# Kernel optimization log

Hardware: AMD Instinct MI355X
Metric: run time of the kernel (lower is better)

Reference implementation:

```python
import jax, jax.numpy as jnp
import numpy as np
from jax import lax

B, DIM, H, W = 8, 128, 64, 64
CQ, DI, DS, RK = 32, 64, 16, 2  # quarter dim, d_inner=2*CQ, d_state, dt_rank=ceil(32/16)
EPS = 1e-5


def _dw(x, w, dil):
    # depthwise conv, x: [B,C,H,W], w: [C,1,kh,kw], torch padding='same'
    return lax.conv_general_dilated(x, w, (1, 1), 'SAME', rhs_dilation=(dil, dil),
                                    dimension_numbers=('NCHW', 'OIHW', 'NCHW'),
                                    feature_group_count=x.shape[1])


def _ln(x, g, b):
    mu = jnp.mean(x, -1, keepdims=True)
    v = jnp.mean((x - mu) ** 2, -1, keepdims=True)
    return (x - mu) * lax.rsqrt(v + EPS) * g + b


def _bn_eval(x, g, b):
    # BatchNorm2d eval mode with default running stats (mean 0, var 1)
    return x * lax.rsqrt(jnp.float32(1.0) + EPS) * g[None, :, None, None] + b[None, :, None, None]


def _axial_dw(x, kh, kw, k3, g, b, dil):
    y = _dw(x, kw, dil)   # (1,w) mixer
    y = _dw(y, kh, dil)   # (h,1) mixer
    y = _dw(y, k3, dil)   # 3x3 dw
    return _bn_eval(y, g, b) + x


def _vss(x, ln_g, ln_b, in_w, conv_w, conv_b, xproj_w, dtw, dtb, A_logs, Ds, on_g, on_b, out_w):
    # x: [B,H,W,CQ] channels-last; VMamba VSSBlock: x + SS2D(LN(x))
    Bb, Hh, Ww, _ = x.shape
    L = Hh * Ww
    xz = _ln(x, ln_g, ln_b) @ in_w.T                      # [B,H,W,2*DI]
    xw, z = jnp.split(xz, 2, axis=-1)
    xc = jax.nn.silu(_dw(xw.transpose(0, 3, 1, 2), conv_w, 1) + conv_b[None, :, None, None])
    xf = xc.reshape(Bb, DI, L)                            # row-major scan
    xwh = xc.transpose(0, 1, 3, 2).reshape(Bb, DI, L)     # column-major scan
    xs = jnp.stack([xf, xwh, jnp.flip(xf, -1), jnp.flip(xwh, -1)], axis=1)  # [B,4,DI,L]
    x_dbl = jnp.einsum('bkdl,kcd->bkcl', xs, xproj_w)     # [B,4,RK+2*DS,L]
    delta = jax.nn.softplus(jnp.einsum('bkrl,kdr->bkdl', x_dbl[:, :, :RK], dtw) + dtb[None, :, :, None])
    Bs, Cs = x_dbl[:, :, RK:RK + DS], x_dbl[:, :, RK + DS:]
    A = -jnp.exp(A_logs)                                  # [4,DI,DS]

    def step(h, t):
        u, d, Bt, Ct = t                                  # u,d:[B,4,DI]; Bt,Ct:[B,4,DS]
        h = h * jnp.exp(d[..., None] * A) + (d * u)[..., None] * Bt[:, :, None, :]
        return h, jnp.einsum('bkdn,bkn->bkd', h, Ct)

    seq = (xs.transpose(3, 0, 1, 2), delta.transpose(3, 0, 1, 2),
           Bs.transpose(3, 0, 1, 2), Cs.transpose(3, 0, 1, 2))
    _, ys = lax.scan(step, jnp.zeros((Bb, 4, DI, DS), x.dtype), seq)  # [L,B,4,DI]
    ys = ys.transpose(1, 2, 3, 0) + Ds[None, :, :, None] * xs         # [B,4,DI,L]
    y = ys[:, 0] + jnp.flip(ys[:, 2], -1)
    y_wh = ys[:, 1] + jnp.flip(ys[:, 3], -1)
    y = y + y_wh.reshape(Bb, DI, Ww, Hh).transpose(0, 1, 3, 2).reshape(Bb, DI, L)
    y = _ln(y.reshape(Bb, DI, Hh, Ww).transpose(0, 2, 3, 1), on_g, on_b)
    return x + (y * jax.nn.silu(z)) @ out_w.T


def _forward(x, dw1_kh, dw1_kw, dw1_k3, dw1_g, dw1_b, dw2_kh, dw2_kw, dw2_k3, dw2_g, dw2_b,
             dw3_kh, dw3_kw, dw3_k3, dw3_g, dw3_b, ln_g, ln_b, in_w, conv_w, conv_b, xproj_w,
             dtw, dtb, A_logs, Ds, on_g, on_b, out_w, scale1, scale2, scale3, scale4, bn_g, bn_b):
    x1, x2, x3, x4 = jnp.split(x, 4, axis=1)
    vp = (ln_g, ln_b, in_w, conv_w, conv_b, xproj_w, dtw, dtb, A_logs, Ds, on_g, on_b, out_w)

    def branch(xi, kh, kw, k3, g, b, dil, s):
        y = _axial_dw(xi, kh, kw, k3, g, b, dil)
        y = _vss(y.transpose(0, 2, 3, 1), *vp).transpose(0, 3, 1, 2)
        return y * s

    y1 = branch(x1, dw1_kh, dw1_kw, dw1_k3, dw1_g, dw1_b, 1, scale1)
    y2 = branch(x2, dw2_kh, dw2_kw, dw2_k3, dw2_g, dw2_b, 2, scale2)
    y3 = branch(x3, dw3_kh, dw3_kw, dw3_k3, dw3_g, dw3_b, 3, scale3)
    y4 = x4 * scale4
    return jax.nn.relu(_bn_eval(jnp.concatenate([y1, y2, y3, y4], 1), bn_g, bn_b))


def setup_inputs():
    ks = jax.random.split(jax.random.key(0), 40)
    rn = lambda k, s, sc: jax.random.normal(k, s, jnp.float32) * sc
    inp = {'x': jax.random.normal(ks[0], (B, DIM, H, W), jnp.float32)}
    for i, n in enumerate(['dw1', 'dw2', 'dw3']):
        inp[n + '_kh'] = rn(ks[1 + 3 * i], (CQ, 1, 7, 1), 0.2)
        inp[n + '_kw'] = rn(ks[2 + 3 * i], (CQ, 1, 1, 7), 0.2)
        inp[n + '_k3'] = rn(ks[3 + 3 * i], (CQ, 1, 3, 3), 0.2)
        inp[n + '_g'] = jnp.ones((CQ,))
        inp[n + '_b'] = jnp.zeros((CQ,))
    inp['ln_g'] = jnp.ones((CQ,))
    inp['ln_b'] = jnp.zeros((CQ,))
    inp['in_w'] = rn(ks[10], (2 * DI, CQ), 0.1)
    inp['conv_w'] = rn(ks[11], (DI, 1, 3, 3), 0.2)
    inp['conv_b'] = jnp.zeros((DI,))
    inp['xproj_w'] = rn(ks[12], (4, RK + 2 * DS, DI), 0.1)
    inp['dtw'] = rn(ks[13], (4, DI, RK), 0.5)
    inp['dtb'] = rn(ks[14], (4, DI), 0.5)
    inp['A_logs'] = jnp.log(jnp.broadcast_to(jnp.arange(1, DS + 1, dtype=jnp.float32), (4, DI, DS)))
    inp['Ds'] = jnp.ones((4, DI))
    inp['on_g'] = jnp.ones((DI,))
    inp['on_b'] = jnp.zeros((DI,))
    inp['out_w'] = rn(ks[15], (CQ, DI), 0.1)
    for n in ['scale1', 'scale2', 'scale3', 'scale4']:
        inp[n] = jnp.ones((1,))
    inp['bn_g'] = jnp.ones((DIM,))
    inp['bn_b'] = jnp.zeros((DIM,))
    return inp


def reference(x, dw1_kh, dw1_kw, dw1_k3, dw1_g, dw1_b, dw2_kh, dw2_kw, dw2_k3, dw2_g, dw2_b,
              dw3_kh, dw3_kw, dw3_k3, dw3_g, dw3_b, ln_g, ln_b, in_w, conv_w, conv_b, xproj_w,
              dtw, dtb, A_logs, Ds, on_g, on_b, out_w, scale1, scale2, scale3, scale4, bn_g, bn_b):
    return _forward(x, dw1_kh, dw1_kw, dw1_k3, dw1_g, dw1_b, dw2_kh, dw2_kw, dw2_k3, dw2_g, dw2_b,
                    dw3_kh, dw3_kw, dw3_k3, dw3_g, dw3_b, ln_g, ln_b, in_w, conv_w, conv_b, xproj_w,
                    dtw, dtb, A_logs, Ds, on_g, on_b, out_w, scale1, scale2, scale3, scale4, bn_g, bn_b)
```

## Files before the change

### kernel.cpp

```cpp
#include <hip/hip_runtime.h>
#include <hip/hip_bf16.h>
#include <cstdint>

typedef unsigned short ushort_t;
typedef float f32x2 __attribute__((ext_vector_type(2)));

__device__ __forceinline__ float softplus2(float x){
    return fmaxf(x, 0.f) + __logf(1.f + __expf(-fabsf(x)));
}
__device__ __forceinline__ float siluf(float x){
    return x / (1.f + __expf(-x));
}
__device__ __forceinline__ float b2f(ushort_t u){
    union { uint32_t i; float f; } v; v.i = ((uint32_t)u)<<16; return v.f;
}
__device__ __forceinline__ ushort_t f2b(float f){
    uint32_t x = __float_as_uint(f);
    uint32_t r = (x + 0x7FFFu + ((x>>16)&1u)) >> 16;
    return (ushort_t)r;
}

struct AxialParams {
    const float* kh[3]; const float* kw[3]; const float* k3[3];
    const float* g[3];  const float* b[3];
};

__global__ __launch_bounds__(256) void k_axial(const float* __restrict__ x,
                                               float* __restrict__ Y0, AxialParams P){
    __shared__ float s0[4096];
    __shared__ float s1[4096];
    int bid = blockIdx.x;
    int i = bid >> 8;
    int rem = bid & 255;
    int b = rem >> 5, c = rem & 31;
    int dil = i + 1;
    const float* xin = x + ((size_t)(b*128 + i*32 + c))*4096;
    float wkw[7], wkh[7], wk3[9];
    #pragma unroll
    for(int t=0;t<7;t++){ wkw[t]=P.kw[i][c*7+t]; wkh[t]=P.kh[i][c*7+t]; }
    #pragma unroll
    for(int t=0;t<9;t++) wk3[t]=P.k3[i][c*9+t];
    float gc = P.g[i][c], bc = P.b[i][c];
    int tid = threadIdx.x;
    for(int idx=tid; idx<4096; idx+=256) s0[idx]=xin[idx];
    __syncthreads();
    for(int idx=tid; idx<4096; idx+=256){
        int h=idx>>6, w=idx&63; float a=0.f;
        #pragma unroll
        for(int t=0;t<7;t++){ int ww=w+(t-3)*dil; if(ww>=0&&ww<64) a=fmaf(s0[h*64+ww],wkw[t],a); }
        s1[idx]=a;
    }
    __syncthreads();
    for(int idx=tid; idx<4096; idx+=256){
        int h=idx>>6, w=idx&63; float a=0.f;
        #pragma unroll
        for(int t=0;t<7;t++){ int hh=h+(t-3)*dil; if(hh>=0&&hh<64) a=fmaf(s1[hh*64+w],wkh[t],a); }
        s0[idx]=a;
    }
    __syncthreads();
    const float inv = rsqrtf(1.00001f);
    float* out = Y0 + ((size_t)(i*8+b)*32 + c)*4096;
    for(int idx=tid; idx<4096; idx+=256){
        int h=idx>>6, w=idx&63; float a=0.f;
        #pragma unroll
        for(int t=0;t<9;t++){
            int hh=h+((t/3)-1)*dil, ww=w+((t%3)-1)*dil;
            if(hh>=0&&hh<64&&ww>=0&&ww<64) a=fmaf(s0[hh*64+ww],wk3[t],a);
        }
        out[idx] = a*inv*gc + bc + xin[idx];
    }
}

__global__ __launch_bounds__(256) void k_lnproj(const float* __restrict__ Y0,
        const float* __restrict__ ln_g, const float* __restrict__ ln_b,
        const float* __restrict__ in_w, ushort_t* __restrict__ XW, ushort_t* __restrict__ ZS){
    __shared__ float W[128*32];
    int tid=threadIdx.x;
    for(int idx=tid; idx<4096; idx+=256) W[idx]=in_w[idx];
    __syncthreads();
    int pg = blockIdx.x*256 + tid;
    int ib = pg>>12, p = pg&4095;
    const float* src = Y0 + (size_t)ib*32*4096;
    float t[32];
    float mu=0.f;
    #pragma unroll
    for(int c=0;c<32;c++){ t[c]=src[c*4096+p]; mu+=t[c]; }
    mu *= (1.f/32.f);
    float v=0.f;
    #pragma unroll
    for(int c=0;c<32;c++){ float d=t[c]-mu; v+=d*d; }
    v *= (1.f/32.f);
    float rs = rsqrtf(v+1e-5f);
    #pragma unroll
    for(int c=0;c<32;c++) t[c] = (t[c]-mu)*rs*ln_g[c] + ln_b[c];
    ushort_t* xw = XW + (size_t)ib*64*4096 + p;
    ushort_t* zs = ZS + (size_t)ib*64*4096 + p;
    for(int j=0;j<64;j++){
        float a=0.f, a2=0.f;
        #pragma unroll
        for(int c=0;c<32;c++){
            a  = fmaf(t[c], W[j*32+c],      a);
            a2 = fmaf(t[c], W[(j+64)*32+c], a2);
        }
        xw[(size_t)j*4096] = f2b(a);
        zs[(size_t)j*4096] = f2b(siluf(a2));
    }
}

__global__ __launch_bounds__(256) void k_dwt(const ushort_t* __restrict__ XW,
        const float* __restrict__ cw, const float* __restrict__ cb,
        ushort_t* __restrict__ XC, ushort_t* __restrict__ XCT){
    __shared__ ushort_t sin_[4096];
    __shared__ ushort_t tr[64*66];
    int bid=blockIdx.x, tid=threadIdx.x;
    int d = bid&63;
    const ushort_t* src = XW + (size_t)bid*4096;
    for(int idx=tid; idx<1024; idx+=256)
        *reinterpret_cast<ushort4*>(&sin_[idx*4]) = *reinterpret_cast<const ushort4*>(&src[idx*4]);
    float wk[9];
    #pragma unroll
    for(int t=0;t<9;t++) wk[t]=cw[d*9+t];
    float bias=cb[d];
    __syncthreads();
    ushort_t* outp = XC + (size_t)bid*4096;
    for(int idx=tid; idx<4096; idx+=256){
        int h=idx>>6, wq=idx&63;
        float a=bias;
        #pragma unroll
        for(int t=0;t<9;t++){
            int hh=h+(t/3)-1, ww=wq+(t%3)-1;
            if(hh>=0&&hh<64&&ww>=0&&ww<64) a=fmaf(b2f(sin_[hh*64+ww]),wk[t],a);
        }
        ushort_t vb = f2b(siluf(a));
        outp[idx]=vb;
        tr[wq*66+h]=vb;
    }
    __syncthreads();
    ushort_t* outt = XCT + (size_t)bid*4096;
    for(int idx=tid; idx<4096; idx+=256){
        outt[idx]=tr[(idx>>6)*66+(idx&63)];
    }
}

__global__ __launch_bounds__(256) void k_transpose(const ushort_t* __restrict__ src, ushort_t* __restrict__ dst){
    __shared__ ushort_t tile[64*66];
    size_t plane = blockIdx.x;
    const ushort_t* s = src + plane*4096;
    ushort_t* d = dst + plane*4096;
    int tid=threadIdx.x;
    for(int idx=tid; idx<4096; idx+=256){
        int h=idx>>6, w=idx&63;
        tile[w*66+h]=s[idx];
    }
    __syncthreads();
    for(int idx=tid; idx<4096; idx+=256){
        d[idx]=tile[(idx>>6)*66 + (idx&63)];
    }
}

__global__ __launch_bounds__(256) void k_xdbl(const ushort_t* __restrict__ XC, const ushort_t* __restrict__ XCT,
        const float* __restrict__ xproj, ushort_t* __restrict__ XBb, ushort_t* __restrict__ XCc,
        float* __restrict__ DT){
    __shared__ float Wt[64][36];
    int bid=blockIdx.x; int tid=threadIdx.x;
    int ibk = bid>>4; int lb = bid&15;
    int k = ibk & 3; int ib = ibk>>2;
    for(int idx=tid; idx<2176; idx+=256){
        int c=idx>>6, dd=idx&63;
        Wt[dd][c]=xproj[k*2176+idx];
    }
    __syncthreads();
    int l = lb*256+tid;
    const ushort_t* src = ((k&1)?XCT:XC) + (size_t)ib*64*4096;
    int idxl = (k&2)? (4095-l) : l;
    float acc[34];
    #pragma unroll
    for(int c=0;c<34;c++) acc[c]=0.f;
    for(int dd=0;dd<64;dd++){
        float u = b2f(src[(size_t)dd*4096 + idxl]);
        float wv[36];
        const float4* wp = reinterpret_cast<const float4*>(&Wt[dd][0]);
        *reinterpret_cast<float4*>(&wv[0])  = wp[0];
        *reinterpret_cast<float4*>(&wv[4])  = wp[1];
        *reinterpret_cast<float4*>(&wv[8])  = wp[2];
        *reinterpret_cast<float4*>(&wv[12]) = wp[3];
        *reinterpret_cast<float4*>(&wv[16]) = wp[4];
        *reinterpret_cast<float4*>(&wv[20]) = wp[5];
        *reinterpret_cast<float4*>(&wv[24]) = wp[6];
        *reinterpret_cast<float4*>(&wv[28]) = wp[7];
        *reinterpret_cast<float2*>(&wv[32]) = *reinterpret_cast<const float2*>(&Wt[dd][32]);
        #pragma unroll
        for(int c=0;c<34;c++) acc[c] = fmaf(u, wv[c], acc[c]);
    }
    DT[((size_t)ibk*2)*4096 + l]   = acc[0];
    DT[((size_t)ibk*2+1)*4096 + l] = acc[1];
    ushort_t* ob = XBb + ((size_t)ibk*16)*4096 + l;
    ushort_t* oc = XCc + ((size_t)ibk*16)*4096 + l;
    #pragma unroll
    for(int c=0;c<16;c++){
        ob[(size_t)c*4096]=f2b(acc[2+c]);
        oc[(size_t)c*4096]=f2b(acc[18+c]);
    }
}


template<bool UNI>
__device__ __forceinline__ void scan1_body(int w,int d,float dt0,float dt1,float db,
    const float* An, f32x2* h2, float& S,
    const float (*sB)[64][16], const float (*sdt)[64][2], const ushort_t (*su)[66])
{
    for(int s=0;s<64;s++){
        const float* dp=&sdt[w][s][0];
        float delta=softplus2(fmaf(dt0,dp[0],fmaf(dt1,dp[1],db)));
        S+=delta;
        int j = w? 63-s : s;
        float du = delta*b2f(su[j][d]);
        float bb[16];
        const float4* bp=reinterpret_cast<const float4*>(&sB[w][s][0]);
        reinterpret_cast<float4*>(bb)[0]=bp[0];
        reinterpret_cast<float4*>(bb)[1]=bp[1];
        reinterpret_cast<float4*>(bb)[2]=bp[2];
        reinterpret_cast<float4*>(bb)[3]=bp[3];
        if(UNI){
            float r1=__expf(delta*An[0]);
            f32x2 a={r1,r1*r1}, rq={r1*r1,r1*r1}, du2={du,du};
            const f32x2* b2p=reinterpret_cast<const f32x2*>(bb);
            #pragma unroll
            for(int i=0;i<8;i++){ h2[i]=h2[i]*a+du2*b2p[i]; a=a*rq; }
        } else {
            float* hf=reinterpret_cast<float*>(h2);
            #pragma unroll
            for(int n=0;n<16;n++){ float a=__expf(delta*An[n]); hf[n]=fmaf(hf[n],a,du*bb[n]); }
        }
    }
}

__global__ __launch_bounds__(128) void k_scan1(const ushort_t* __restrict__ XBb, const float* __restrict__ DT,
        const ushort_t* __restrict__ XC, const ushort_t* __restrict__ XCT,
        const float* __restrict__ dtw, const float* __restrict__ dtb,
        const float* __restrict__ A_logs,
        ushort_t* __restrict__ CHS, float* __restrict__ SD){
    __shared__ float sB[2][64][16];
    __shared__ float sdt[2][64][2];
    __shared__ ushort_t su[64][66];
    int bid=blockIdx.x, tid=threadIdx.x;
    int ib = bid>>7; int rem = bid&127; int p = rem>>6; int ch = rem&63;
    int w = tid>>6, d = tid&63;
    int l0 = ch*64, r0 = 4032 - l0;
    const ushort_t* B0 = XBb + (size_t)(4*ib+p)*16*4096;
    const ushort_t* B1 = XBb + (size_t)(4*ib+p+2)*16*4096;
    for(int idx=tid; idx<512; idx+=128){
        int w2=idx>>8, n=(idx>>4)&15, q=(idx&15)*4;
        const ushort_t* Bs = w2? B1 : B0;
        int base = (w2? r0 : l0) + q;
        ushort4 v = *reinterpret_cast<const ushort4*>(&Bs[(size_t)n*4096 + base]);
        sB[w2][q+0][n]=b2f(v.x); sB[w2][q+1][n]=b2f(v.y); sB[w2][q+2][n]=b2f(v.z); sB[w2][q+3][n]=b2f(v.w);
    }
    {
        const float* D0 = DT + (size_t)(4*ib+p)*2*4096;
        const float* D1 = DT + (size_t)(4*ib+p+2)*2*4096;
        int r=tid>>6, s=tid&63;
        sdt[0][s][r] = D0[(size_t)r*4096 + l0 + s];
        sdt[1][s][r] = D1[(size_t)r*4096 + r0 + s];
    }
    const ushort_t* U = (p?XCT:XC) + (size_t)ib*64*4096;
    for(int idx=tid; idx<1024; idx+=128){
        int r=idx>>4, q=(idx&15)*4;
        ushort4 v = *reinterpret_cast<const ushort4*>(&U[(size_t)r*4096 + l0 + q]);
        su[q+0][r]=v.x; su[q+1][r]=v.y; su[q+2][r]=v.z; su[q+3][r]=v.w;
    }
    __syncthreads();
    int k = p + 2*w;
    float dt0=dtw[(k*64+d)*2], dt1=dtw[(k*64+d)*2+1], db=dtb[k*64+d];
    float An[16];
    #pragma unroll
    for(int n=0;n<16;n++) An[n] = -__expf(A_logs[(k*64+d)*16+n]);
    bool st = true;
    #pragma unroll
    for(int n=1;n<16;n++) st = st && (fabsf(An[n]-(n+1)*An[0]) <= 1e-4f*fabsf(An[n]) + 1e-6f);
    bool uni = (bool)__all((int)st);
    f32x2 h2[8];
    #pragma unroll
    for(int i=0;i<8;i++){ h2[i].x=0.f; h2[i].y=0.f; }
    float S=0.f;
    if(uni) scan1_body<true >(w,d,dt0,dt1,db,An,h2,S,sB,sdt,su);
    else    scan1_body<false>(w,d,dt0,dt1,db,An,h2,S,sB,sdt,su);
    int chd = w ? 63-ch : ch;
    ushort_t* o = CHS + ((size_t)(4*ib+k)*64 + chd)*1024 + d*16;
    const float* hf = reinterpret_cast<const float*>(h2);
    #pragma unroll
    for(int n=0;n<16;n++) o[n]=f2b(hf[n]);
    SD[((size_t)(4*ib+k)*64 + chd)*64 + d]=S;
}

__global__ __launch_bounds__(1024) void k_scan2(const float* __restrict__ A_logs,
        const float* __restrict__ SD, ushort_t* __restrict__ CHS){
    __shared__ float sS[4096];
    int ibk=blockIdx.x; int tid=threadIdx.x;
    for(int idx=tid; idx<4096; idx+=1024) sS[idx]=SD[(size_t)ibk*4096+idx];
    __syncthreads();
    int d=tid>>4, n=tid&15, k=ibk&3;
    float An = -__expf(A_logs[(k*64+d)*16+n]);
    float H=0.f;
    for(int c=0;c<64;c++){
        float pc = __expf(An*sS[c*64+d]);
        size_t o = ((size_t)ibk*64+c)*1024 + tid;
        float loc = b2f(CHS[o]);
        CHS[o]=f2b(H);
        H = fmaf(H, pc, loc);
    }
}

__device__ __forceinline__ const ushort_t* seg_src(int idx, int seg,
        const ushort_t* B0, const ushort_t* B1, const ushort_t* C0, const ushort_t* C1,
        int l0, int r0){
    int arr=idx>>8, w2=(idx>>7)&1, n=(idx>>3)&15, qi=idx&7;
    const ushort_t* S = arr? (w2?C1:C0) : (w2?B1:B0);
    int base = (w2? r0 : l0) + seg*32 + qi*4;
    return &S[(size_t)n*4096 + base];
}
__device__ __forceinline__ void seg_wr(int idx, ushort4 v,
        float (*sB)[32][16], float (*sC)[32][16]){
    int arr=idx>>8, w2=(idx>>7)&1, n=(idx>>3)&15, qi=idx&7;
    float (*dst)[32][16] = arr? sC : sB;
    int sl=qi*4;
    dst[w2][sl+0][n]=b2f(v.x); dst[w2][sl+1][n]=b2f(v.y);
    dst[w2][sl+2][n]=b2f(v.z); dst[w2][sl+3][n]=b2f(v.w);
}

template<bool UNI, int SEG>
__device__ __forceinline__ void scan3_seg(int w,int d,float dt0,float dt1,float db,
    const float* An, f32x2* h2,
    const float (*sB)[32][16], const float (*sC)[32][16],
    const float (*sdt)[64][2], const ushort_t (*su)[66], ushort_t (*sy)[66])
{
    for(int t=0;t<32;t++){
        int s = SEG*32 + t;
        const float* dp=&sdt[w][s][0];
        float delta=softplus2(fmaf(dt0,dp[0],fmaf(dt1,dp[1],db)));
        int j = w? 63-s : s;
        float du = delta*b2f(su[j][d]);
        float bb[16], cc[16];
        const float4* bp=reinterpret_cast<const float4*>(&sB[w][t][0]);
        const float4* cp=reinterpret_cast<const float4*>(&sC[w][t][0]);
        reinterpret_cast<float4*>(bb)[0]=bp[0]; reinterpret_cast<float4*>(bb)[1]=bp[1];
        reinterpret_cast<float4*>(bb)[2]=bp[2]; reinterpret_cast<float4*>(bb)[3]=bp[3];
        reinterpret_cast<float4*>(cc)[0]=cp[0]; reinterpret_cast<float4*>(cc)[1]=cp[1];
        reinterpret_cast<float4*>(cc)[2]=cp[2]; reinterpret_cast<float4*>(cc)[3]=cp[3];
        float y;
        if(UNI){
            float r1=__expf(delta*An[0]);
            f32x2 a={r1,r1*r1}, rq={r1*r1,r1*r1}, du2={du,du};
            f32x2 y2={0.f,0.f};
            const f32x2* b2p=reinterpret_cast<const f32x2*>(bb);
            const f32x2* c2p=reinterpret_cast<const f32x2*>(cc);
            #pragma unroll
            for(int i=0;i<8;i++){
                h2[i]=h2[i]*a+du2*b2p[i];
                y2=y2+h2[i]*c2p[i];
                a=a*rq;
            }
            y = y2.x + y2.y;
        } else {
            y=0.f;
            float* hf=reinterpret_cast<float*>(h2);
            #pragma unroll
            for(int n=0;n<16;n++){
                float a=__expf(delta*An[n]);
                hf[n]=fmaf(hf[n],a,du*bb[n]);
                y=fmaf(hf[n],cc[n],y);
            }
        }
        if(SEG==0) sy[j][d]=f2b(y);
        else       sy[j][d]=f2b(b2f(sy[j][d])+y);
    }
}

__global__ __launch_bounds__(128) void k_scan3(const ushort_t* __restrict__ XBb, const ushort_t* __restrict__ XCc,
        const float* __restrict__ DT,
        const ushort_t* __restrict__ XC, const ushort_t* __restrict__ XCT,
        const float* __restrict__ dtw, const float* __restrict__ dtb,
        const float* __restrict__ A_logs,
        const ushort_t* __restrict__ CHS,
        ushort_t* __restrict__ Y1, ushort_t* __restrict__ Y2){
    __shared__ float sB[2][32][16];
    __shared__ float sC[2][32][16];
    __shared__ float sdt[2][64][2];
    __shared__ ushort_t su[64][66];
    __shared__ ushort_t sy[64][66];
    int bid=blockIdx.x, tid=threadIdx.x;
    int ib = bid>>7; int rem = bid&127; int p = rem>>6; int ch = rem&63;
    int w = tid>>6, d = tid&63;
    int l0 = ch*64, r0 = 4032 - l0;
    const ushort_t* B0 = XBb + (size_t)(4*ib+p)*16*4096;
    const ushort_t* B1 = XBb + (size_t)(4*ib+p+2)*16*4096;
    const ushort_t* C0 = XCc + (size_t)(4*ib+p)*16*4096;
    const ushort_t* C1 = XCc + (size_t)(4*ib+p+2)*16*4096;
    for(int idx=tid; idx<512; idx+=128)
        seg_wr(idx, *reinterpret_cast<const ushort4*>(seg_src(idx,0,B0,B1,C0,C1,l0,r0)), sB, sC);
    {
        const float* D0 = DT + (size_t)(4*ib+p)*2*4096;
        const float* D1 = DT + (size_t)(4*ib+p+2)*2*4096;
        int r=tid>>6, s=tid&63;
        sdt[0][s][r] = D0[(size_t)r*4096 + l0 + s];
        sdt[1][s][r] = D1[(size_t)r*4096 + r0 + s];
    }
    const ushort_t* U = (p?XCT:XC) + (size_t)ib*64*4096;
    for(int idx=tid; idx<1024; idx+=128){
        int r=idx>>4, q=(idx&15)*4;
        ushort4 v = *reinterpret_cast<const ushort4*>(&U[(size_t)r*4096 + l0 + q]);
        su[q+0][r]=v.x; su[q+1][r]=v.y; su[q+2][r]=v.z; su[q+3][r]=v.w;
    }
    __syncthreads();
    ushort4 pf[4];
    #pragma unroll
    for(int r=0;r<4;r++)
        pf[r] = *reinterpret_cast<const ushort4*>(seg_src(tid+r*128,1,B0,B1,C0,C1,l0,r0));
    int k = p + 2*w;
    float dt0=dtw[(k*64+d)*2], dt1=dtw[(k*64+d)*2+1], db=dtb[k*64+d];
    float An[16];
    #pragma unroll
    for(int n=0;n<16;n++) An[n] = -__expf(A_logs[(k*64+d)*16+n]);
    bool st = true;
    #pragma unroll
    for(int n=1;n<16;n++) st = st && (fabsf(An[n]-(n+1)*An[0]) <= 1e-4f*fabsf(An[n]) + 1e-6f);
    bool uni = (bool)__all((int)st);
    int chd = w ? 63-ch : ch;
    const ushort_t* e = CHS + ((size_t)(4*ib+k)*64 + chd)*1024 + d*16;
    f32x2 h2[8];
    {
        float* hf = reinterpret_cast<float*>(h2);
        #pragma unroll
        for(int n=0;n<16;n++) hf[n]=b2f(e[n]);
    }
    if(uni) scan3_seg<true ,0>(w,d,dt0,dt1,db,An,h2,sB,sC,sdt,su,sy);
    else    scan3_seg<false,0>(w,d,dt0,dt1,db,An,h2,sB,sC,sdt,su,sy);
    __syncthreads();
    #pragma unroll
    for(int r=0;r<4;r++) seg_wr(tid+r*128, pf[r], sB, sC);
    __syncthreads();
    if(uni) scan3_seg<true ,1>(w,d,dt0,dt1,db,An,h2,sB,sC,sdt,su,sy);
    else    scan3_seg<false,1>(w,d,dt0,dt1,db,An,h2,sB,sC,sdt,su,sy);
    __syncthreads();
    ushort_t* Yb = (p?Y2:Y1) + (size_t)ib*64*4096;
    for(int idx=tid; idx<1024; idx+=128){
        int r=idx>>4, q=(idx&15)*4;
        ushort4 v;
        v.x=sy[q+0][r]; v.y=sy[q+1][r]; v.z=sy[q+2][r]; v.w=sy[q+3][r];
        *reinterpret_cast<ushort4*>(&Yb[(size_t)r*4096 + l0 + q]) = v;
    }
}

__global__ __launch_bounds__(256) void k_final(const ushort_t* __restrict__ Y1, const ushort_t* __restrict__ Y2T,
        const ushort_t* __restrict__ ZS, const float* __restrict__ Y0,
        const ushort_t* __restrict__ XC, const float* __restrict__ Ds,
        const float* __restrict__ on_g, const float* __restrict__ on_b,
        const float* __restrict__ out_w,
        const float* __restrict__ s1, const float* __restrict__ s2, const float* __restrict__ s3,
        const float* __restrict__ bn_g, const float* __restrict__ bn_b,
        float* __restrict__ out){
    __shared__ float W[32*64];
    __shared__ float sD[64];
    int tid=threadIdx.x;
    for(int idx=tid; idx<2048; idx+=256) W[idx]=out_w[idx];
    if(tid<64) sD[tid]=Ds[tid]+Ds[64+tid]+Ds[128+tid]+Ds[192+tid];
    __syncthreads();
    int pg=blockIdx.x*256+tid;
    int ib=pg>>12, p=pg&4095;
    int i=ib>>3, b=ib&7;
    float y[64];
    const ushort_t* y1 = Y1 + (size_t)ib*64*4096 + p;
    const ushort_t* y2 = Y2T + (size_t)ib*64*4096 + p;
    const ushort_t* xc = XC + (size_t)ib*64*4096 + p;
    float mu=0.f;
    #pragma unroll
    for(int dd=0;dd<64;dd++){
        y[dd]=b2f(y1[(size_t)dd*4096])+b2f(y2[(size_t)dd*4096])+sD[dd]*b2f(xc[(size_t)dd*4096]);
        mu+=y[dd];
    }
    mu*=(1.f/64.f);
    float v=0.f;
    #pragma unroll
    for(int dd=0;dd<64;dd++){ float q=y[dd]-mu; v+=q*q; }
    v*=(1.f/64.f);
    float rs=rsqrtf(v+1e-5f);
    const ushort_t* zs = ZS + (size_t)ib*64*4096 + p;
    #pragma unroll
    for(int dd=0;dd<64;dd++){
        float yn=(y[dd]-mu)*rs*on_g[dd]+on_b[dd];
        y[dd]=yn*b2f(zs[(size_t)dd*4096]);
    }
    float sc = (i==0)?s1[0]:((i==1)?s2[0]:s3[0]);
    const float inv = rsqrtf(1.00001f);
    const float* y0 = Y0 + (size_t)ib*32*4096 + p;
    for(int c=0;c<32;c++){
        float a=0.f;
        #pragma unroll
        for(int dd=0;dd<64;dd++) a=fmaf(y[dd],W[c*64+dd],a);
        float o=(y0[(size_t)c*4096]+a)*sc;
        int chn=i*32+c;
        float vv=fmaf(o*inv, bn_g[chn], bn_b[chn]);
        out[((size_t)b*128+chn)*4096 + p]=fmaxf(vv,0.f);
    }
}

__global__ __launch_bounds__(256) void k_branch4(const float* __restrict__ x,
        const float* __restrict__ s4, const float* __restrict__ bn_g,
        const float* __restrict__ bn_b, float* __restrict__ out){
    int g=blockIdx.x*256+threadIdx.x;
    int b=g>>17; int rem=g&131071; int c=rem>>12; int p=rem&4095;
    int chn=96+c;
    const float inv=rsqrtf(1.00001f);
    float v=x[((size_t)b*128+chn)*4096+p]*s4[0];
    v=fmaf(v*inv, bn_g[chn], bn_b[chn]);
    out[((size_t)b*128+chn)*4096+p]=fmaxf(v,0.f);
}

extern "C" void kernel_launch(void* const* d_in, const int* in_sizes, int n_in,
                              void* d_out, int out_size, void* d_ws, size_t ws_size,
                              hipStream_t stream) {
    const float* x      = (const float*)d_in[0];
    const float* ln_g   = (const float*)d_in[16];
    const float* ln_b   = (const float*)d_in[17];
    const float* in_w   = (const float*)d_in[18];
    const float* conv_w = (const float*)d_in[19];
    const float* conv_b = (const float*)d_in[20];
    const float* xproj  = (const float*)d_in[21];
    const float* dtw    = (const float*)d_in[22];
    const float* dtb    = (const float*)d_in[23];
    const float* A_logs = (const float*)d_in[24];
    const float* Ds     = (const float*)d_in[25];
    const float* on_g   = (const float*)d_in[26];
    const float* on_b   = (const float*)d_in[27];
    const float* out_w  = (const float*)d_in[28];
    const float* sc1    = (const float*)d_in[29];
    const float* sc2    = (const float*)d_in[30];
    const float* sc3    = (const float*)d_in[31];
    const float* sc4    = (const float*)d_in[32];
    const float* bn_g   = (const float*)d_in[33];
    const float* bn_b   = (const float*)d_in[34];

    AxialParams P;
    for(int i=0;i<3;i++){
        P.kh[i]=(const float*)d_in[1+5*i];
        P.kw[i]=(const float*)d_in[2+5*i];
        P.k3[i]=(const float*)d_in[3+5*i];
        P.g[i] =(const float*)d_in[4+5*i];
        P.b[i] =(const float*)d_in[5+5*i];
    }

    char* base = (char*)d_ws;
    float*    Y0   = (float*)   (base + 0);
    ushort_t* ZS   = (ushort_t*)(base + 12582912);
    ushort_t* XC   = (ushort_t*)(base + 25165824);
    ushort_t* XCT  = (ushort_t*)(base + 37748736);
    ushort_t* XBb  = (ushort_t*)(base + 50331648);
    ushort_t* XW   = (ushort_t*)(base + 50331648);
    ushort_t* XCc  = (ushort_t*)(base + 62914560);
    float*    DT   = (float*)   (base + 75497472);
    ushort_t* CHS  = (ushort_t*)(base + 78643200);
    float*    SD   = (float*)   (base + 91226112);
    ushort_t* Y1   = (ushort_t*)(base + 92798976);
    ushort_t* Y2   = (ushort_t*)(base + 105381888);
    ushort_t* Y2T  = XBb;

    float* out = (float*)d_out;

    k_axial    <<<768,   256, 0, stream>>>(x, Y0, P);
    k_lnproj   <<<384,   256, 0, stream>>>(Y0, ln_g, ln_b, in_w, XW, ZS);
    k_dwt      <<<1536,  256, 0, stream>>>(XW, conv_w, conv_b, XC, XCT);
    k_xdbl     <<<1536,  256, 0, stream>>>(XC, XCT, xproj, XBb, XCc, DT);
    k_scan1    <<<3072,  128, 0, stream>>>(XBb, DT, XC, XCT, dtw, dtb, A_logs, CHS, SD);
    k_scan2    <<<96,   1024, 0, stream>>>(A_logs, SD, CHS);
    k_scan3    <<<3072,  128, 0, stream>>>(XBb, XCc, DT, XC, XCT, dtw, dtb, A_logs, CHS, Y1, Y2);
    k_transpose<<<1536,  256, 0, stream>>>(Y2, Y2T);
    k_final    <<<384,   256, 0, stream>>>(Y1, Y2T, ZS, Y0, XC, Ds, on_g, on_b, out_w,
                                           sc1, sc2, sc3, bn_g, bn_b, out);
    k_branch4  <<<4096,  256, 0, stream>>>(x, sc4, bn_g, bn_b, out);
}
```

Before: 286.6 us.

## Shrink scan chunks, share xdbl input tile across directions, drop transpose kernel

k_xdbl now loads a 64x128 input tile into shared memory once and computes both the forward and reversed scan directions from it. The chunked scan halves its chunk length to 32, doubling block count and carry entries, and k_scan2 now walks 128 chunks. k_scan3 writes its outputs position-major into a combined buffer, writing the column scan already transposed, so the separate transpose kernel goes away and k_final2 reads contiguous per-pixel vectors. The intent is to cut redundant global reads and one kernel launch plus its traffic, at the cost of a longer sequential carry pass and scattered writes for the transposed direction.

```diff
diff --git a/kernel.cpp b/kernel.cpp
--- a/kernel.cpp
+++ b/kernel.cpp
@@ -142,64 +142,58 @@
     }
 }
 
-__global__ __launch_bounds__(256) void k_transpose(const ushort_t* __restrict__ src, ushort_t* __restrict__ dst){
-    __shared__ ushort_t tile[64*66];
-    size_t plane = blockIdx.x;
-    const ushort_t* s = src + plane*4096;
-    ushort_t* d = dst + plane*4096;
-    int tid=threadIdx.x;
-    for(int idx=tid; idx<4096; idx+=256){
-        int h=idx>>6, w=idx&63;
-        tile[w*66+h]=s[idx];
-    }
-    __syncthreads();
-    for(int idx=tid; idx<4096; idx+=256){
-        d[idx]=tile[(idx>>6)*66 + (idx&63)];
-    }
-}
-
-__global__ __launch_bounds__(256) void k_xdbl(const ushort_t* __restrict__ XC, const ushort_t* __restrict__ XCT,
+__global__ __launch_bounds__(128) void k_xdbl(const ushort_t* __restrict__ XC, const ushort_t* __restrict__ XCT,
         const float* __restrict__ xproj, ushort_t* __restrict__ XBb, ushort_t* __restrict__ XCc,
         float* __restrict__ DT){
+    __shared__ ushort_t tile[64][128];
     __shared__ float Wt[64][36];
-    int bid=blockIdx.x; int tid=threadIdx.x;
-    int ibk = bid>>4; int lb = bid&15;
-    int k = ibk & 3; int ib = ibk>>2;
-    for(int idx=tid; idx<2176; idx+=256){
-        int c=idx>>6, dd=idx&63;
-        Wt[dd][c]=xproj[k*2176+idx];
-    }
-    __syncthreads();
-    int l = lb*256+tid;
-    const ushort_t* src = ((k&1)?XCT:XC) + (size_t)ib*64*4096;
-    int idxl = (k&2)? (4095-l) : l;
-    float acc[34];
-    #pragma unroll
-    for(int c=0;c<34;c++) acc[c]=0.f;
-    for(int dd=0;dd<64;dd++){
-        float u = b2f(src[(size_t)dd*4096 + idxl]);
-        float wv[36];
-        const float4* wp = reinterpret_cast<const float4*>(&Wt[dd][0]);
-        *reinterpret_cast<float4*>(&wv[0])  = wp[0];
-        *reinterpret_cast<float4*>(&wv[4])  = wp[1];
-        *reinterpret_cast<float4*>(&wv[8])  = wp[2];
-        *reinterpret_cast<float4*>(&wv[12]) = wp[3];
-        *reinterpret_cast<float4*>(&wv[16]) = wp[4];
-        *reinterpret_cast<float4*>(&wv[20]) = wp[5];
-        *reinterpret_cast<float4*>(&wv[24]) = wp[6];
-        *reinterpret_cast<float4*>(&wv[28]) = wp[7];
-        *reinterpret_cast<float2*>(&wv[32]) = *reinterpret_cast<const float2*>(&Wt[dd][32]);
-        #pragma unroll
-        for(int c=0;c<34;c++) acc[c] = fmaf(u, wv[c], acc[c]);
-    }
-    DT[((size_t)ibk*2)*4096 + l]   = acc[0];
-    DT[((size_t)ibk*2+1)*4096 + l] = acc[1];
-    ushort_t* ob = XBb + ((size_t)ibk*16)*4096 + l;
-    ushort_t* oc = XCc + ((size_t)ibk*16)*4096 + l;
-    #pragma unroll
-    for(int c=0;c<16;c++){
-        ob[(size_t)c*4096]=f2b(acc[2+c]);
-        oc[(size_t)c*4096]=f2b(acc[18+c]);
+    int bid=blockIdx.x, tid=threadIdx.x;
+    int lb = bid&31, t=(bid>>5)&1, ib=bid>>6;
+    int m0 = lb*128;
+    const ushort_t* src = (t?XCT:XC) + (size_t)ib*64*4096;
+    for(int idx=tid; idx<2048; idx+=128){
+        int dd=idx>>5, q=(idx&31)*4;
+        *reinterpret_cast<ushort4*>(&tile[dd][q]) =
+            *reinterpret_cast<const ushort4*>(&src[(size_t)dd*4096 + m0 + q]);
+    }
+    int m = m0 + tid;
+    for(int pass=0; pass<2; ++pass){
+        int k = t + 2*pass;
+        __syncthreads();
+        for(int idx=tid; idx<2176; idx+=128){
+            int c=idx>>6, dd=idx&63;
+            Wt[dd][c]=xproj[k*2176+idx];
+        }
+        __syncthreads();
+        float acc[34];
+        #pragma unroll
+        for(int c=0;c<34;c++) acc[c]=0.f;
+        for(int dd=0;dd<64;dd++){
+            float u = b2f(tile[dd][tid]);
+            float wv[36];
+            const float4* wp = reinterpret_cast<const float4*>(&Wt[dd][0]);
+            *reinterpret_cast<float4*>(&wv[0])  = wp[0];
+            *reinterpret_cast<float4*>(&wv[4])  = wp[1];
+            *reinterpret_cast<float4*>(&wv[8])  = wp[2];
+            *reinterpret_cast<float4*>(&wv[12]) = wp[3];
+            *reinterpret_cast<float4*>(&wv[16]) = wp[4];
+            *reinterpret_cast<float4*>(&wv[20]) = wp[5];
+            *reinterpret_cast<float4*>(&wv[24]) = wp[6];
+            *reinterpret_cast<float4*>(&wv[28]) = wp[7];
+            *reinterpret_cast<float2*>(&wv[32]) = *reinterpret_cast<const float2*>(&Wt[dd][32]);
+            #pragma unroll
+            for(int c=0;c<34;c++) acc[c] = fmaf(u, wv[c], acc[c]);
+        }
+        int l = pass ? (4095-m) : m;
+        DT[((size_t)(ib*4+k)*2)*4096 + l]   = acc[0];
+        DT[((size_t)(ib*4+k)*2+1)*4096 + l] = acc[1];
+        ushort_t* ob = XBb + ((size_t)(ib*4+k)*16)*4096 + l;
+        ushort_t* oc = XCc + ((size_t)(ib*4+k)*16)*4096 + l;
+        #pragma unroll
+        for(int c=0;c<16;c++){
+            ob[(size_t)c*4096]=f2b(acc[2+c]);
+            oc[(size_t)c*4096]=f2b(acc[18+c]);
+        }
     }
 }
 
@@ -207,16 +201,16 @@
 template<bool UNI>
 __device__ __forceinline__ void scan1_body(int w,int d,float dt0,float dt1,float db,
     const float* An, f32x2* h2, float& S,
-    const float (*sB)[64][16], const float (*sdt)[64][2], const ushort_t (*su)[66])
+    const float (*sB)[32][16], const float (*sdt)[32][2], const ushort_t (*su)[66])
 {
-    for(int s=0;s<64;s++){
-        const float* dp=&sdt[w][s][0];
+    for(int t=0;t<32;t++){
+        const float* dp=&sdt[w][t][0];
         float delta=softplus2(fmaf(dt0,dp[0],fmaf(dt1,dp[1],db)));
         S+=delta;
-        int j = w? 63-s : s;
+        int j = w? 31-t : t;
         float du = delta*b2f(su[j][d]);
         float bb[16];
-        const float4* bp=reinterpret_cast<const float4*>(&sB[w][s][0]);
+        const float4* bp=reinterpret_cast<const float4*>(&sB[w][t][0]);
         reinterpret_cast<float4*>(bb)[0]=bp[0];
         reinterpret_cast<float4*>(bb)[1]=bp[1];
         reinterpret_cast<float4*>(bb)[2]=bp[2];
@@ -240,32 +234,33 @@
         const float* __restrict__ dtw, const float* __restrict__ dtb,
         const float* __restrict__ A_logs,
         ushort_t* __restrict__ CHS, float* __restrict__ SD){
-    __shared__ float sB[2][64][16];
-    __shared__ float sdt[2][64][2];
-    __shared__ ushort_t su[64][66];
+    __shared__ float sB[2][32][16];
+    __shared__ float sdt[2][32][2];
+    __shared__ ushort_t su[32][66];
     int bid=blockIdx.x, tid=threadIdx.x;
-    int ib = bid>>7; int rem = bid&127; int p = rem>>6; int ch = rem&63;
+    int ib = bid>>8; int rem = bid&255; int p = rem>>7; int ch = rem&127;
     int w = tid>>6, d = tid&63;
-    int l0 = ch*64, r0 = 4032 - l0;
+    int l0 = ch*32, r0 = 4064 - l0;
     const ushort_t* B0 = XBb + (size_t)(4*ib+p)*16*4096;
     const ushort_t* B1 = XBb + (size_t)(4*ib+p+2)*16*4096;
-    for(int idx=tid; idx<512; idx+=128){
-        int w2=idx>>8, n=(idx>>4)&15, q=(idx&15)*4;
-        const ushort_t* Bs = w2? B1 : B0;
-        int base = (w2? r0 : l0) + q;
-        ushort4 v = *reinterpret_cast<const ushort4*>(&Bs[(size_t)n*4096 + base]);
-        sB[w2][q+0][n]=b2f(v.x); sB[w2][q+1][n]=b2f(v.y); sB[w2][q+2][n]=b2f(v.z); sB[w2][q+3][n]=b2f(v.w);
+    for(int idx=tid; idx<256; idx+=128){
+        int n=idx&15, qi=(idx>>4)&7, w2=idx>>7;
+        int base=(w2? r0 : l0) + qi*4;
+        ushort4 v = *reinterpret_cast<const ushort4*>(&(w2?B1:B0)[(size_t)n*4096 + base]);
+        int sl=qi*4;
+        sB[w2][sl+0][n]=b2f(v.x); sB[w2][sl+1][n]=b2f(v.y);
+        sB[w2][sl+2][n]=b2f(v.z); sB[w2][sl+3][n]=b2f(v.w);
     }
     {
         const float* D0 = DT + (size_t)(4*ib+p)*2*4096;
         const float* D1 = DT + (size_t)(4*ib+p+2)*2*4096;
-        int r=tid>>6, s=tid&63;
-        sdt[0][s][r] = D0[(size_t)r*4096 + l0 + s];
-        sdt[1][s][r] = D1[(size_t)r*4096 + r0 + s];
+        int w2=tid>>6; int rem2=tid&63; int s=rem2>>1; int r=rem2&1;
+        sdt[w2][s][r]      = (w2? D1 : D0)[(size_t)r*4096 + (w2? r0 : l0) + s];
+        sdt[w2][s+16][r]   = (w2? D1 : D0)[(size_t)r*4096 + (w2? r0 : l0) + s + 16];
     }
     const ushort_t* U = (p?XCT:XC) + (size_t)ib*64*4096;
-    for(int idx=tid; idx<1024; idx+=128){
-        int r=idx>>4, q=(idx&15)*4;
+    for(int idx=tid; idx<512; idx+=128){
+        int r=idx>>3, q=(idx&7)*4;
         ushort4 v = *reinterpret_cast<const ushort4*>(&U[(size_t)r*4096 + l0 + q]);
         su[q+0][r]=v.x; su[q+1][r]=v.y; su[q+2][r]=v.z; su[q+3][r]=v.w;
     }
@@ -285,60 +280,43 @@
     float S=0.f;
     if(uni) scan1_body<true >(w,d,dt0,dt1,db,An,h2,S,sB,sdt,su);
     else    scan1_body<false>(w,d,dt0,dt1,db,An,h2,S,sB,sdt,su);
-    int chd = w ? 63-ch : ch;
-    ushort_t* o = CHS + ((size_t)(4*ib+k)*64 + chd)*1024 + d*16;
+    int chd = w ? 127-ch : ch;
+    ushort_t* o = CHS + ((size_t)(4*ib+k)*128 + chd)*1024 + d*16;
     const float* hf = reinterpret_cast<const float*>(h2);
     #pragma unroll
     for(int n=0;n<16;n++) o[n]=f2b(hf[n]);
-    SD[((size_t)(4*ib+k)*64 + chd)*64 + d]=S;
+    SD[((size_t)(4*ib+k)*128 + chd)*64 + d]=S;
 }
 
 __global__ __launch_bounds__(1024) void k_scan2(const float* __restrict__ A_logs,
         const float* __restrict__ SD, ushort_t* __restrict__ CHS){
-    __shared__ float sS[4096];
+    __shared__ float sS[8192];
     int ibk=blockIdx.x; int tid=threadIdx.x;
-    for(int idx=tid; idx<4096; idx+=1024) sS[idx]=SD[(size_t)ibk*4096+idx];
+    for(int idx=tid; idx<8192; idx+=1024) sS[idx]=SD[(size_t)ibk*8192+idx];
     __syncthreads();
     int d=tid>>4, n=tid&15, k=ibk&3;
     float An = -__expf(A_logs[(k*64+d)*16+n]);
     float H=0.f;
-    for(int c=0;c<64;c++){
+    for(int c=0;c<128;c++){
         float pc = __expf(An*sS[c*64+d]);
-        size_t o = ((size_t)ibk*64+c)*1024 + tid;
+        size_t o = ((size_t)ibk*128+c)*1024 + tid;
         float loc = b2f(CHS[o]);
         CHS[o]=f2b(H);
         H = fmaf(H, pc, loc);
     }
 }
 
-__device__ __forceinline__ const ushort_t* seg_src(int idx, int seg,
-        const ushort_t* B0, const ushort_t* B1, const ushort_t* C0, const ushort_t* C1,
-        int l0, int r0){
-    int arr=idx>>8, w2=(idx>>7)&1, n=(idx>>3)&15, qi=idx&7;
-    const ushort_t* S = arr? (w2?C1:C0) : (w2?B1:B0);
-    int base = (w2? r0 : l0) + seg*32 + qi*4;
-    return &S[(size_t)n*4096 + base];
-}
-__device__ __forceinline__ void seg_wr(int idx, ushort4 v,
-        float (*sB)[32][16], float (*sC)[32][16]){
-    int arr=idx>>8, w2=(idx>>7)&1, n=(idx>>3)&15, qi=idx&7;
-    float (*dst)[32][16] = arr? sC : sB;
-    int sl=qi*4;
-    dst[w2][sl+0][n]=b2f(v.x); dst[w2][sl+1][n]=b2f(v.y);
-    dst[w2][sl+2][n]=b2f(v.z); dst[w2][sl+3][n]=b2f(v.w);
-}
-
-template<bool UNI, int SEG>
-__device__ __forceinline__ void scan3_seg(int w,int d,float dt0,float dt1,float db,
-    const float* An, f32x2* h2,
+template<bool UNI, bool ADD>
+__device__ __forceinline__ void scan3_phase(int w,int d,float dt0,float dt1,float db,
+    const float* An, f32x2* h2, int T0,
     const float (*sB)[32][16], const float (*sC)[32][16],
-    const float (*sdt)[64][2], const ushort_t (*su)[66], ushort_t (*sy)[66])
+    const float (*sdt)[32][2], const ushort_t (*su)[66], ushort_t (*sy)[66])
 {
-    for(int t=0;t<32;t++){
-        int s = SEG*32 + t;
-        const float* dp=&sdt[w][s][0];
+    for(int tt=0;tt<16;tt++){
+        int t = T0 + tt;
+        const float* dp=&sdt[w][t][0];
         float delta=softplus2(fmaf(dt0,dp[0],fmaf(dt1,dp[1],db)));
-        int j = w? 63-s : s;
+        int j = w? 31-t : t;
         float du = delta*b2f(su[j][d]);
         float bb[16], cc[16];
         const float4* bp=reinterpret_cast<const float4*>(&sB[w][t][0]);
@@ -371,8 +349,8 @@
                 y=fmaf(hf[n],cc[n],y);
             }
         }
-        if(SEG==0) sy[j][d]=f2b(y);
-        else       sy[j][d]=f2b(b2f(sy[j][d])+y);
+        if(ADD) sy[j][d]=f2b(b2f(sy[j][d])+y);
+        else    sy[j][d]=f2b(y);
     }
 }
 
@@ -382,40 +360,44 @@
         const float* __restrict__ dtw, const float* __restrict__ dtb,
         const float* __restrict__ A_logs,
         const ushort_t* __restrict__ CHS,
-        ushort_t* __restrict__ Y1, ushort_t* __restrict__ Y2){
+        ushort_t* __restrict__ YS){
     __shared__ float sB[2][32][16];
     __shared__ float sC[2][32][16];
-    __shared__ float sdt[2][64][2];
-    __shared__ ushort_t su[64][66];
-    __shared__ ushort_t sy[64][66];
+    __shared__ float sdt[2][32][2];
+    __shared__ ushort_t su[32][66];
+    __shared__ ushort_t sy[32][66];
     int bid=blockIdx.x, tid=threadIdx.x;
-    int ib = bid>>7; int rem = bid&127; int p = rem>>6; int ch = rem&63;
+    int ib = bid>>8; int rem = bid&255; int p = rem>>7; int ch = rem&127;
     int w = tid>>6, d = tid&63;
-    int l0 = ch*64, r0 = 4032 - l0;
+    int l0 = ch*32, r0 = 4064 - l0;
     const ushort_t* B0 = XBb + (size_t)(4*ib+p)*16*4096;
     const ushort_t* B1 = XBb + (size_t)(4*ib+p+2)*16*4096;
     const ushort_t* C0 = XCc + (size_t)(4*ib+p)*16*4096;
     const ushort_t* C1 = XCc + (size_t)(4*ib+p+2)*16*4096;
-    for(int idx=tid; idx<512; idx+=128)
-        seg_wr(idx, *reinterpret_cast<const ushort4*>(seg_src(idx,0,B0,B1,C0,C1,l0,r0)), sB, sC);
+    for(int idx=tid; idx<512; idx+=128){
+        int n=idx&15, qi=(idx>>4)&7, w2=(idx>>7)&1, arr=idx>>8;
+        int base=(w2? r0 : l0) + qi*4;
+        const ushort_t* S = arr? (w2?C1:C0) : (w2?B1:B0);
+        ushort4 v = *reinterpret_cast<const ushort4*>(&S[(size_t)n*4096 + base]);
+        float (*dst)[32][16] = arr? sC : sB;
+        int sl=qi*4;
+        dst[w2][sl+0][n]=b2f(v.x); dst[w2][sl+1][n]=b2f(v.y);
+        dst[w2][sl+2][n]=b2f(v.z); dst[w2][sl+3][n]=b2f(v.w);
+    }
     {
         const float* D0 = DT + (size_t)(4*ib+p)*2*4096;
         const float* D1 = DT + (size_t)(4*ib+p+2)*2*4096;
-        int r=tid>>6, s=tid&63;
-        sdt[0][s][r] = D0[(size_t)r*4096 + l0 + s];
-        sdt[1][s][r] = D1[(size_t)r*4096 + r0 + s];
+        int w2=tid>>6; int rem2=tid&63; int s=rem2>>1; int r=rem2&1;
+        sdt[w2][s][r]      = (w2? D1 : D0)[(size_t)r*4096 + (w2? r0 : l0) + s];
+        sdt[w2][s+16][r]   = (w2? D1 : D0)[(size_t)r*4096 + (w2? r0 : l0) + s + 16];
     }
     const ushort_t* U = (p?XCT:XC) + (size_t)ib*64*4096;
-    for(int idx=tid; idx<1024; idx+=128){
-        int r=idx>>4, q=(idx&15)*4;
+    for(int idx=tid; idx<512; idx+=128){
+        int r=idx>>3, q=(idx&7)*4;
         ushort4 v = *reinterpret_cast<const ushort4*>(&U[(size_t)r*4096 + l0 + q]);
         su[q+0][r]=v.x; su[q+1][r]=v.y; su[q+2][r]=v.z; su[q+3][r]=v.w;
     }
     __syncthreads();
-    ushort4 pf[4];
-    #pragma unroll
-    for(int r=0;r<4;r++)
-        pf[r] = *reinterpret_cast<const ushort4*>(seg_src(tid+r*128,1,B0,B1,C0,C1,l0,r0));
     int k = p + 2*w;
     float dt0=dtw[(k*64+d)*2], dt1=dtw[(k*64+d)*2+1], db=dtb[k*64+d];
     float An[16];
@@ -425,33 +407,40 @@
     #pragma unroll
     for(int n=1;n<16;n++) st = st && (fabsf(An[n]-(n+1)*An[0]) <= 1e-4f*fabsf(An[n]) + 1e-6f);
     bool uni = (bool)__all((int)st);
-    int chd = w ? 63-ch : ch;
-    const ushort_t* e = CHS + ((size_t)(4*ib+k)*64 + chd)*1024 + d*16;
+    int chd = w ? 127-ch : ch;
+    const ushort_t* e = CHS + ((size_t)(4*ib+k)*128 + chd)*1024 + d*16;
     f32x2 h2[8];
     {
         float* hf = reinterpret_cast<float*>(h2);
         #pragma unroll
         for(int n=0;n<16;n++) hf[n]=b2f(e[n]);
     }
-    if(uni) scan3_seg<true ,0>(w,d,dt0,dt1,db,An,h2,sB,sC,sdt,su,sy);
-    else    scan3_seg<false,0>(w,d,dt0,dt1,db,An,h2,sB,sC,sdt,su,sy);
-    __syncthreads();
-    #pragma unroll
-    for(int r=0;r<4;r++) seg_wr(tid+r*128, pf[r], sB, sC);
-    __syncthreads();
-    if(uni) scan3_seg<true ,1>(w,d,dt0,dt1,db,An,h2,sB,sC,sdt,su,sy);
-    else    scan3_seg<false,1>(w,d,dt0,dt1,db,An,h2,sB,sC,sdt,su,sy);
-    __syncthreads();
-    ushort_t* Yb = (p?Y2:Y1) + (size_t)ib*64*4096;
-    for(int idx=tid; idx<1024; idx+=128){
-        int r=idx>>4, q=(idx&15)*4;
-        ushort4 v;
-        v.x=sy[q+0][r]; v.y=sy[q+1][r]; v.z=sy[q+2][r]; v.w=sy[q+3][r];
-        *reinterpret_cast<ushort4*>(&Yb[(size_t)r*4096 + l0 + q]) = v;
-    }
-}
-
-__global__ __launch_bounds__(256) void k_final(const ushort_t* __restrict__ Y1, const ushort_t* __restrict__ Y2T,
+    if(uni) scan3_phase<true ,false>(w,d,dt0,dt1,db,An,h2, 0,sB,sC,sdt,su,sy);
+    else    scan3_phase<false,false>(w,d,dt0,dt1,db,An,h2, 0,sB,sC,sdt,su,sy);
+    __syncthreads();
+    if(uni) scan3_phase<true ,true >(w,d,dt0,dt1,db,An,h2,16,sB,sC,sdt,su,sy);
+    else    scan3_phase<false,true >(w,d,dt0,dt1,db,An,h2,16,sB,sC,sdt,su,sy);
+    __syncthreads();
+    ushort_t* plane = YS + (size_t)(ib*2+p)*262144;
+    if(p==0){
+        for(int idx=tid; idx<512; idx+=128){
+            int jr=idx>>4, q=(idx&15)*4;
+            ushort4 v;
+            v.x=sy[jr][q+0]; v.y=sy[jr][q+1]; v.z=sy[jr][q+2]; v.w=sy[jr][q+3];
+            *reinterpret_cast<ushort4*>(&plane[(size_t)(l0+jr)*64 + q]) = v;
+        }
+    } else {
+        int hi = l0>>6, lo0 = l0&63;
+        for(int idx=tid; idx<512; idx+=128){
+            int jr=idx>>4, q=(idx&15)*4;
+            ushort4 v;
+            v.x=sy[jr][q+0]; v.y=sy[jr][q+1]; v.z=sy[jr][q+2]; v.w=sy[jr][q+3];
+            *reinterpret_cast<ushort4*>(&plane[(size_t)(lo0+jr)*4096 + hi*64 + q]) = v;
+        }
+    }
+}
+
+__global__ __launch_bounds__(256) void k_final2(const ushort_t* __restrict__ YS,
         const ushort_t* __restrict__ ZS, const float* __restrict__ Y0,
         const ushort_t* __restrict__ XC, const float* __restrict__ Ds,
         const float* __restrict__ on_g, const float* __restrict__ on_b,
@@ -468,15 +457,28 @@
     int pg=blockIdx.x*256+tid;
     int ib=pg>>12, p=pg&4095;
     int i=ib>>3, b=ib&7;
+    const ushort_t* r0p = YS + (size_t)(ib*2+0)*262144 + (size_t)p*64;
+    const ushort_t* r1p = YS + (size_t)(ib*2+1)*262144 + (size_t)p*64;
+    const ushort_t* xc = XC + (size_t)ib*64*4096 + p;
     float y[64];
-    const ushort_t* y1 = Y1 + (size_t)ib*64*4096 + p;
-    const ushort_t* y2 = Y2T + (size_t)ib*64*4096 + p;
-    const ushort_t* xc = XC + (size_t)ib*64*4096 + p;
     float mu=0.f;
     #pragma unroll
-    for(int dd=0;dd<64;dd++){
-        y[dd]=b2f(y1[(size_t)dd*4096])+b2f(y2[(size_t)dd*4096])+sD[dd]*b2f(xc[(size_t)dd*4096]);
-        mu+=y[dd];
+    for(int qq=0; qq<8; ++qq){
+        ushort4 a0 = reinterpret_cast<const ushort4*>(r0p)[qq*2];
+        ushort4 b0 = reinterpret_cast<const ushort4*>(r0p)[qq*2+1];
+        ushort4 a1 = reinterpret_cast<const ushort4*>(r1p)[qq*2];
+        ushort4 b1 = reinterpret_cast<const ushort4*>(r1p)[qq*2+1];
+        const ushort_t* u0=reinterpret_cast<const ushort_t*>(&a0);
+        const ushort_t* u1=reinterpret_cast<const ushort_t*>(&b0);
+        const ushort_t* v0=reinterpret_cast<const ushort_t*>(&a1);
+        const ushort_t* v1=reinterpret_cast<const ushort_t*>(&b1);
+        #pragma unroll
+        for(int e=0;e<4;e++){
+            int dd=qq*8+e;
+            y[dd]   = b2f(u0[e])+b2f(v0[e]) + sD[dd]  *b2f(xc[(size_t)dd*4096]);
+            y[dd+4] = b2f(u1[e])+b2f(v1[e]) + sD[dd+4]*b2f(xc[(size_t)(dd+4)*4096]);
+            mu += y[dd]+y[dd+4];
+        }
     }
     mu*=(1.f/64.f);
     float v=0.f;
@@ -559,22 +561,19 @@
     ushort_t* XCc  = (ushort_t*)(base + 62914560);
     float*    DT   = (float*)   (base + 75497472);
     ushort_t* CHS  = (ushort_t*)(base + 78643200);
-    float*    SD   = (float*)   (base + 91226112);
-    ushort_t* Y1   = (ushort_t*)(base + 92798976);
-    ushort_t* Y2   = (ushort_t*)(base + 105381888);
-    ushort_t* Y2T  = XBb;
+    float*    SD   = (float*)   (base + 103809024);
+    ushort_t* YS   = (ushort_t*)(base + 106954752);
 
     float* out = (float*)d_out;
 
     k_axial    <<<768,   256, 0, stream>>>(x, Y0, P);
     k_lnproj   <<<384,   256, 0, stream>>>(Y0, ln_g, ln_b, in_w, XW, ZS);
     k_dwt      <<<1536,  256, 0, stream>>>(XW, conv_w, conv_b, XC, XCT);
-    k_xdbl     <<<1536,  256, 0, stream>>>(XC, XCT, xproj, XBb, XCc, DT);
-    k_scan1    <<<3072,  128, 0, stream>>>(XBb, DT, XC, XCT, dtw, dtb, A_logs, CHS, SD);
+    k_xdbl     <<<1536,  128, 0, stream>>>(XC, XCT, xproj, XBb, XCc, DT);
+    k_scan1    <<<6144,  128, 0, stream>>>(XBb, DT, XC, XCT, dtw, dtb, A_logs, CHS, SD);
     k_scan2    <<<96,   1024, 0, stream>>>(A_logs, SD, CHS);
-    k_scan3    <<<3072,  128, 0, stream>>>(XBb, XCc, DT, XC, XCT, dtw, dtb, A_logs, CHS, Y1, Y2);
-    k_transpose<<<1536,  256, 0, stream>>>(Y2, Y2T);
-    k_final    <<<384,   256, 0, stream>>>(Y1, Y2T, ZS, Y0, XC, Ds, on_g, on_b, out_w,
+    k_scan3    <<<6144,  128, 0, stream>>>(XBb, XCc, DT, XC, XCT, dtw, dtb, A_logs, CHS, YS);
+    k_final2   <<<384,   256, 0, stream>>>(YS, ZS, Y0, XC, Ds, on_g, on_b, out_w,
                                            sc1, sc2, sc3, bn_g, bn_b, out);
     k_branch4  <<<4096,  256, 0, stream>>>(x, sc4, bn_g, bn_b, out);
 }
```

Result: slower. 308.8 us (+7.7%).
